# Kernel optimization log

Hardware: AMD Instinct MI355X
Metric: run time of the kernel (lower is better)

## Reference

```python
import jax, jax.numpy as jnp
import numpy as np

N = 100000   # nodes
E = 1600000  # edges (before self-loops)
G = 64       # graphs in batch
IN = 8
H = 4        # heads
EPS_BN = 1e-5

def setup_inputs() -> dict:
    key = jax.random.key(0)
    ks = jax.random.split(key, 30)
    def nrm(k, shape, s=0.1):
        return jax.random.normal(k, shape, dtype=jnp.float32) * s
    inp = {}
    inp['x'] = nrm(ks[0], (N, IN), 1.0)
    inp['edge_index'] = jax.random.randint(ks[1], (2, E), 0, N)
    inp['batch'] = jnp.sort(jax.random.randint(ks[2], (N,), 0, G))
    # GATConv 1: 8 -> 64, 4 heads (concat=False)
    inp['W1'] = nrm(ks[3], (IN, H * 64)); inp['aS1'] = nrm(ks[4], (H, 64)); inp['aD1'] = nrm(ks[5], (H, 64)); inp['b1'] = jnp.zeros((64,), jnp.float32)
    inp['g1'] = jnp.ones((64,), jnp.float32); inp['be1'] = jnp.zeros((64,), jnp.float32)
    # GATConv 2: 64 -> 64
    inp['W2'] = nrm(ks[6], (64, H * 64)); inp['aS2'] = nrm(ks[7], (H, 64)); inp['aD2'] = nrm(ks[8], (H, 64)); inp['b2'] = jnp.zeros((64,), jnp.float32)
    inp['g2'] = jnp.ones((64,), jnp.float32); inp['be2'] = jnp.zeros((64,), jnp.float32)
    # GATConv 3: 64 -> 32
    inp['W3'] = nrm(ks[9], (64, H * 32)); inp['aS3'] = nrm(ks[10], (H, 32)); inp['aD3'] = nrm(ks[11], (H, 32)); inp['b3'] = jnp.zeros((32,), jnp.float32)
    inp['g3'] = jnp.ones((32,), jnp.float32); inp['be3'] = jnp.zeros((32,), jnp.float32)
    # predictor MLP 32 -> 16 -> 1
    inp['Wp1'] = nrm(ks[12], (32, 16)); inp['bp1'] = jnp.zeros((16,), jnp.float32)
    inp['Wp2'] = nrm(ks[13], (16, 1)); inp['bp2'] = jnp.zeros((1,), jnp.float32)
    return inp

def gat_layer(x, src, dst, W, a_src, a_dst, bias, D):
    # x: [N, Fin]; src/dst: [E'] (self-loops included). PyG GATConv semantics.
    h = (x @ W).reshape(N, H, D)                       # [N,H,D]
    alpha_s = jnp.einsum('nhd,hd->nh', h, a_src)       # [N,H]
    alpha_d = jnp.einsum('nhd,hd->nh', h, a_dst)
    e = jax.nn.leaky_relu(alpha_s[src] + alpha_d[dst], 0.2)  # [E',H]
    # segment softmax over incoming edges of each target node
    m = jax.ops.segment_max(e, dst, num_segments=N)
    e = jnp.exp(e - m[dst])
    s = jax.ops.segment_sum(e, dst, num_segments=N)
    alpha = e / (s[dst] + 1e-16)                       # [E',H]
    out = jax.ops.segment_sum(h[src] * alpha[:, :, None], dst, num_segments=N)  # [N,H,D]
    return out.mean(axis=1) + bias                     # concat=False -> head mean

def batch_norm(x, gamma, beta):
    m = x.mean(0)
    v = x.var(0)
    return (x - m) * jax.lax.rsqrt(v + EPS_BN) * gamma + beta

def reference(x, edge_index, batch,
              W1, aS1, aD1, b1, g1, be1,
              W2, aS2, aD2, b2, g2, be2,
              W3, aS3, aD3, b3, g3, be3,
              Wp1, bp1, Wp2, bp2):
    loop = jnp.arange(N)
    src = jnp.concatenate([edge_index[0], loop])  # add self loops (PyG default)
    dst = jnp.concatenate([edge_index[1], loop])
    h = jax.nn.relu(gat_layer(x, src, dst, W1, aS1, aD1, b1, 64))
    h = batch_norm(h, g1, be1)
    h = jax.nn.relu(gat_layer(h, src, dst, W2, aS2, aD2, b2, 64))
    h = batch_norm(h, g2, be2)
    h = jax.nn.relu(gat_layer(h, src, dst, W3, aS3, aD3, b3, 32))
    h = batch_norm(h, g3, be3)
    # global mean pool over graphs
    cnt = jax.ops.segment_sum(jnp.ones((N,), h.dtype), batch, num_segments=G)
    pooled = jax.ops.segment_sum(h, batch, num_segments=G) / jnp.maximum(cnt, 1.0)[:, None]
    hid = jax.nn.relu(pooled @ Wp1 + bp1)
    return hid @ Wp2 + bp2  # [G,1]
```

## Files before the change

kernel.cpp:

```cpp
#include <hip/hip_runtime.h>
#include <hip/hip_fp16.h>

#define N_NODES 100000
#define N_EDGES 1600000
#define EP (N_EDGES + N_NODES)
#define NG 64
#define NH 4
#define POOL_NPB 256
#define BSHIFT 7
#define BNODES 128
#define NBUCK 782
#define BCAP 3072
#define BCHUNK 4096

static inline int cdiv(int a, int b) { return (a + b - 1) / b; }

typedef _Float16 half8 __attribute__((ext_vector_type(8)));
typedef float f32x4 __attribute__((ext_vector_type(4)));

__device__ __forceinline__ float lrelu(float x) { return x >= 0.f ? x : 0.2f * x; }

__global__ __launch_bounds__(256) void k_bucket(const int* __restrict__ ei,
                                                int* __restrict__ gCursor,
                                                unsigned int* __restrict__ pairs) {
  __shared__ int cnt[NBUCK];
  __shared__ int base[NBUCK];
  int tid = threadIdx.x;
  for (int b = tid; b < NBUCK; b += 256) cnt[b] = 0;
  __syncthreads();
  int e0 = blockIdx.x * BCHUNK;
  unsigned int stV[16];
  int stB[16];
#pragma unroll
  for (int i = 0; i < 16; i++) {
    int e = e0 + i * 256 + tid;
    stB[i] = -1;
    if (e < EP) {
      int d, s;
      if (e < N_EDGES) {
        d = __builtin_nontemporal_load(&ei[N_EDGES + e]);
        s = __builtin_nontemporal_load(&ei[e]);
      } else {
        d = s = e - N_EDGES;
      }
      int b = d >> BSHIFT;
      stV[i] = ((unsigned int)s << BSHIFT) | (unsigned int)(d & (BNODES - 1));
      stB[i] = b;
      atomicAdd(&cnt[b], 1);
    }
  }
  __syncthreads();
  for (int b = tid; b < NBUCK; b += 256) {
    base[b] = atomicAdd(&gCursor[b], cnt[b]);
    cnt[b] = 0;
  }
  __syncthreads();
#pragma unroll
  for (int i = 0; i < 16; i++) {
    if (stB[i] >= 0) {
      int r = atomicAdd(&cnt[stB[i]], 1);
      pairs[base[stB[i]] + r] = stV[i];
    }
  }
}

__global__ __launch_bounds__(1024) void k_bscan(const int* __restrict__ gCursor,
                                                int* __restrict__ bstart) {
  __shared__ int sh[1024];
  int t = threadIdx.x;
  int v = (t < NBUCK) ? (gCursor[t] - t * BCAP) : 0;
  sh[t] = v;
  __syncthreads();
  for (int off = 1; off < 1024; off <<= 1) {
    int add = (t >= off) ? sh[t - off] : 0;
    __syncthreads();
    sh[t] += add;
    __syncthreads();
  }
  if (t < NBUCK) {
    bstart[t] = sh[t] - v;
    if (t == NBUCK - 1) bstart[NBUCK] = sh[t];
  }
}

__global__ __launch_bounds__(256) void k_build(const unsigned int* __restrict__ pairs,
                                               const int* __restrict__ bstart,
                                               int* __restrict__ indptr, int* __restrict__ esrc) {
  __shared__ int cnt[BNODES];
  __shared__ int exc[BNODES];
  __shared__ int ptr[BNODES];
  __shared__ int eLds[BCAP];
  int b = blockIdx.x;
  int tid = threadIdx.x;
  int obase = bstart[b];
  int nE = bstart[b + 1] - obase;
  int pbase = b * BCAP;
  if (tid < BNODES) cnt[tid] = 0;
  __syncthreads();
  unsigned int stV[12];
#pragma unroll
  for (int i = 0; i < 12; i++) {
    int idx = i * 256 + tid;
    stV[i] = 0xFFFFFFFFu;
    if (idx < nE) {
      unsigned int v = pairs[pbase + idx];
      stV[i] = v;
      atomicAdd(&cnt[v & (BNODES - 1)], 1);
    }
  }
  __syncthreads();
  if (tid < BNODES) ptr[tid] = cnt[tid];
  __syncthreads();
  for (int off = 1; off < BNODES; off <<= 1) {
    int add = (tid < BNODES && tid >= off) ? ptr[tid - off] : 0;
    __syncthreads();
    if (tid < BNODES) ptr[tid] += add;
    __syncthreads();
  }
  if (tid < BNODES) {
    exc[tid] = ptr[tid] - cnt[tid];
    int n = (b << BSHIFT) + tid;
    if (n < N_NODES) indptr[n] = obase + exc[tid];
    cnt[tid] = 0;
  }
  if (b == NBUCK - 1 && tid == 0) indptr[N_NODES] = bstart[NBUCK];
  __syncthreads();
#pragma unroll
  for (int i = 0; i < 12; i++) {
    if (stV[i] != 0xFFFFFFFFu) {
      int ln = stV[i] & (BNODES - 1);
      int r = atomicAdd(&cnt[ln], 1);
      eLds[exc[ln] + r] = (int)(stV[i] >> BSHIFT);
    }
  }
  __syncthreads();
  for (int idx = tid; idx < nE; idx += 256) esrc[obase + idx] = eLds[idx];
}

template <int FIN, int D>
__device__ void wvec_impl(const float* __restrict__ W, const float* __restrict__ aS,
                          const float* __restrict__ aD, float* __restrict__ wS,
                          float* __restrict__ wD, int t) {
  if (t >= 4 * FIN) return;
  int h = t / FIN, k = t % FIN;
  float ss = 0.f, dd = 0.f;
  for (int d = 0; d < D; d++) {
    float w = W[k * (4 * D) + h * D + d];
    ss = fmaf(w, aS[h * D + d], ss);
    dd = fmaf(w, aD[h * D + d], dd);
  }
  wS[h * FIN + k] = ss;
  wD[h * FIN + k] = dd;
}

template <int D>
__device__ void wcvt_frag(const float* __restrict__ W, __half* __restrict__ wf, int frag, int l) {
  constexpr int NCT = D / 16;
  int kt = frag / NCT, ct = frag % NCT;
  half8 v;
#pragma unroll
  for (int j = 0; j < 8; j++) {
    int kk = kt * 32 + (l >> 4) * 8 + j;
    int k = kk >> 2, h = kk & 3;
    v[j] = (_Float16)W[k * (4 * D) + h * D + ct * 16 + (l & 15)];
  }
  *(half8*)(wf + (size_t)frag * 512 + l * 8) = v;
}

__global__ __launch_bounds__(256) void k_prep(const float* W1, const float* aS1, const float* aD1,
                                              const float* W2, const float* aS2, const float* aD2,
                                              const float* W3, const float* aS3, const float* aD3,
                                              float* wS1, float* wD1, float* wS2, float* wD2,
                                              float* wS3, float* wD3,
                                              __half* wf1, __half* wf2, __half* wf3,
                                              int* gCursor) {
  int b = blockIdx.x, t = threadIdx.x;
  int f = t >> 6, l = t & 63;
  if (b == 0) wvec_impl<8, 64>(W1, aS1, aD1, wS1, wD1, t);
  else if (b == 1) wvec_impl<64, 64>(W2, aS2, aD2, wS2, wD2, t);
  else if (b == 2) wvec_impl<64, 32>(W3, aS3, aD3, wS3, wD3, t);
  else if (b == 3) wcvt_frag<64>(W1, wf1, f, l);
  else if (b < 12) wcvt_frag<64>(W2, wf2, (b - 4) * 4 + f, l);
  else if (b < 16) wcvt_frag<32>(W3, wf3, (b - 12) * 4 + f, l);
  else {
    int idx = (b - 16) * 256 + t;
    if (idx < NBUCK) gCursor[idx] = idx * BCAP;
  }
}

__global__ void k_attdots1(const float* __restrict__ x, const float* __restrict__ wS,
                           const float* __restrict__ wD, float4* __restrict__ as4,
                           float4* __restrict__ ad4) {
  int n = blockIdx.x * blockDim.x + threadIdx.x;
  if (n >= N_NODES) return;
  float4 s = {0, 0, 0, 0}, d = {0, 0, 0, 0};
#pragma unroll
  for (int k = 0; k < 8; k++) {
    float xv = x[(size_t)n * 8 + k];
    s.x = fmaf(xv, wS[k], s.x);
    s.y = fmaf(xv, wS[8 + k], s.y);
    s.z = fmaf(xv, wS[16 + k], s.z);
    s.w = fmaf(xv, wS[24 + k], s.w);
    d.x = fmaf(xv, wD[k], d.x);
    d.y = fmaf(xv, wD[8 + k], d.y);
    d.z = fmaf(xv, wD[16 + k], d.z);
    d.w = fmaf(xv, wD[24 + k], d.w);
  }
  as4[n] = s;
  ad4[n] = d;
}

__global__ __launch_bounds__(256) void k_bnx(const float* __restrict__ tbuf,
                                             const float* __restrict__ scale,
                                             const float* __restrict__ shift,
                                             const float* __restrict__ wS,
                                             const float* __restrict__ wD,
                                             __half* __restrict__ xhat,
                                             float4* __restrict__ as4, float4* __restrict__ ad4) {
  int lane = threadIdx.x & 63;
  int n = blockIdx.x * 4 + (threadIdx.x >> 6);
  if (n >= N_NODES) return;
  float v = fmaf(tbuf[(size_t)n * 64 + lane], scale[lane], shift[lane]);
  xhat[(size_t)n * 64 + lane] = __float2half(v);
  float p0 = v * wS[lane], p1 = v * wS[64 + lane], p2 = v * wS[128 + lane], p3 = v * wS[192 + lane];
  float q0 = v * wD[lane], q1 = v * wD[64 + lane], q2 = v * wD[128 + lane], q3 = v * wD[192 + lane];
#pragma unroll
  for (int off = 32; off; off >>= 1) {
    p0 += __shfl_xor(p0, off); p1 += __shfl_xor(p1, off);
    p2 += __shfl_xor(p2, off); p3 += __shfl_xor(p3, off);
    q0 += __shfl_xor(q0, off); q1 += __shfl_xor(q1, off);
    q2 += __shfl_xor(q2, off); q3 += __shfl_xor(q3, off);
  }
  if (lane == 0) {
    as4[n] = make_float4(p0, p1, p2, p3);
    ad4[n] = make_float4(q0, q1, q2, q3);
  }
}

template <int DIN, typename TX, int GSH>
__global__ __launch_bounds__(256) void k_agg(const int* __restrict__ indptr,
                                             const int* __restrict__ esrc,
                                             const TX* __restrict__ xg,
                                             const float4* __restrict__ as4,
                                             const float4* __restrict__ ad4,
                                             __half* __restrict__ accO) {
  constexpr int GL = 1 << GSH;
  constexpr int NPW = 64 >> GSH;
  constexpr int DPL = DIN / GL;
  constexpr int SH = (sizeof(TX) == 2) ? 7 : 5;
  constexpr int WB = NPW * (GL + 1);
  __shared__ int sOff[4 * WB];
  __shared__ float4 sW[4 * WB];
  int tid = threadIdx.x;
  int lane = tid & 63;
  int wv = tid >> 6;
  int q = lane & (GL - 1);
  int g = lane >> GSH;
  int n = blockIdx.x * (4 * NPW) + wv * NPW + g;
  if (n >= N_NODES) return;
  int e0 = indptr[n], e1 = indptr[n + 1];
  float4 ad = ad4[n];
  int lbase = wv * WB + g * (GL + 1);
  const char* xb = (const char*)xg + q * DPL * (int)sizeof(TX);
  float s0 = 0.f, s1 = 0.f, s2 = 0.f, s3 = 0.f;
  float a[DPL][4];
#pragma unroll
  for (int d = 0; d < DPL; d++)
#pragma unroll
    for (int h = 0; h < 4; h++) a[d][h] = 0.f;

  for (int c = e0; c < e1; c += GL) {
    int nc = min(GL, e1 - c);
    float w0 = 0.f, w1 = 0.f, w2 = 0.f, w3 = 0.f;
    int sB = 0;
    if (q < nc) {
      int sidx = esrc[c + q];
      float4 av = as4[sidx];
      w0 = __expf(lrelu(av.x + ad.x));
      w1 = __expf(lrelu(av.y + ad.y));
      w2 = __expf(lrelu(av.z + ad.z));
      w3 = __expf(lrelu(av.w + ad.w));
      sB = sidx << SH;
    }
    s0 += w0; s1 += w1; s2 += w2; s3 += w3;
    sOff[lbase + q] = sB;
    sW[lbase + q] = make_float4(w0, w1, w2, w3);
    __builtin_amdgcn_wave_barrier();
    for (int i = 0; i < nc; ++i) {
      float4 w = sW[lbase + i];
      int ob = sOff[lbase + i];
      if constexpr (DPL == 4) {
        uint2 px = *(const uint2*)(xb + ob);
        float2 f01 = __half22float2(*(const __half2*)&px.x);
        float2 f23 = __half22float2(*(const __half2*)&px.y);
        a[0][0] = fmaf(w.x, f01.x, a[0][0]); a[0][1] = fmaf(w.y, f01.x, a[0][1]);
        a[0][2] = fmaf(w.z, f01.x, a[0][2]); a[0][3] = fmaf(w.w, f01.x, a[0][3]);
        a[1][0] = fmaf(w.x, f01.y, a[1][0]); a[1][1] = fmaf(w.y, f01.y, a[1][1]);
        a[1][2] = fmaf(w.z, f01.y, a[1][2]); a[1][3] = fmaf(w.w, f01.y, a[1][3]);
        a[2][0] = fmaf(w.x, f23.x, a[2][0]); a[2][1] = fmaf(w.y, f23.x, a[2][1]);
        a[2][2] = fmaf(w.z, f23.x, a[2][2]); a[2][3] = fmaf(w.w, f23.x, a[2][3]);
        a[3][0] = fmaf(w.x, f23.y, a[3][0]); a[3][1] = fmaf(w.y, f23.y, a[3][1]);
        a[3][2] = fmaf(w.z, f23.y, a[3][2]); a[3][3] = fmaf(w.w, f23.y, a[3][3]);
      } else {
        float xv = *(const float*)(xb + ob);
        a[0][0] = fmaf(w.x, xv, a[0][0]);
        a[0][1] = fmaf(w.y, xv, a[0][1]);
        a[0][2] = fmaf(w.z, xv, a[0][2]);
        a[0][3] = fmaf(w.w, xv, a[0][3]);
      }
    }
    __builtin_amdgcn_wave_barrier();
  }
#pragma unroll
  for (int off = 1; off < GL; off <<= 1) {
    s0 += __shfl_xor(s0, off);
    s1 += __shfl_xor(s1, off);
    s2 += __shfl_xor(s2, off);
    s3 += __shfl_xor(s3, off);
  }
  float r0 = 1.f / (s0 + 1e-16f), r1 = 1.f / (s1 + 1e-16f);
  float r2 = 1.f / (s2 + 1e-16f), r3 = 1.f / (s3 + 1e-16f);
  if constexpr (DPL == 4) {
    __half2 p[8];
#pragma unroll
    for (int d = 0; d < 4; d++) {
      p[2 * d] = __floats2half2_rn(a[d][0] * r0, a[d][1] * r1);
      p[2 * d + 1] = __floats2half2_rn(a[d][2] * r2, a[d][3] * r3);
    }
    uint4 lo = make_uint4(*(unsigned*)&p[0], *(unsigned*)&p[1], *(unsigned*)&p[2], *(unsigned*)&p[3]);
    uint4 hi = make_uint4(*(unsigned*)&p[4], *(unsigned*)&p[5], *(unsigned*)&p[6], *(unsigned*)&p[7]);
    *(uint4*)(accO + (size_t)n * 256 + q * 16) = lo;
    *(uint4*)(accO + (size_t)n * 256 + q * 16 + 8) = hi;
  } else {
    __half2 p01 = __floats2half2_rn(a[0][0] * r0, a[0][1] * r1);
    __half2 p23 = __floats2half2_rn(a[0][2] * r2, a[0][3] * r3);
    uint2 pk = make_uint2(*(unsigned*)&p01, *(unsigned*)&p23);
    *(uint2*)(accO + (size_t)n * 32 + q * 4) = pk;
  }
}

template <int DOUT, int NK>
__global__ __launch_bounds__(256) void k_post_mfma(const __half* __restrict__ accA,
                                                   const __half* __restrict__ wfrag,
                                                   const float* __restrict__ bias,
                                                   float* __restrict__ tbuf) {
  constexpr int NCT = DOUT / 16;
  constexpr int AS = NK * 32;
  int l = threadIdx.x & 63;
  int n0 = (blockIdx.x * 4 + (threadIdx.x >> 6)) * 16;
  int m = l & 15, kg = l >> 4;
  f32x4 c[NCT];
#pragma unroll
  for (int ct = 0; ct < NCT; ct++) c[ct] = (f32x4){0.f, 0.f, 0.f, 0.f};
#pragma unroll
  for (int kt = 0; kt < NK; kt++) {
    half8 a = *(const half8*)(accA + (size_t)(n0 + m) * AS + kt * 32 + kg * 8);
#pragma unroll
    for (int ct = 0; ct < NCT; ct++) {
      half8 b = *(const half8*)(wfrag + ((kt * NCT + ct) * 64 + l) * 8);
      c[ct] = __builtin_amdgcn_mfma_f32_16x16x32_f16(a, b, c[ct], 0, 0, 0);
    }
  }
#pragma unroll
  for (int ct = 0; ct < NCT; ct++) {
    float bv = bias[ct * 16 + m];
#pragma unroll
    for (int j = 0; j < 4; j++) {
      int n = n0 + kg * 4 + j;
      if (n < N_NODES) tbuf[(size_t)n * DOUT + ct * 16 + m] = fmaxf(fmaf(c[ct][j], 0.25f, bv), 0.f);
    }
  }
}

template <int C>
__global__ __launch_bounds__(256) void k_bnstat(const float* __restrict__ x, float* __restrict__ part) {
  const int RG = 256 / C;
  int col = threadIdx.x & (C - 1);
  int rg = threadIdx.x / C;
  int rows = (N_NODES + gridDim.x - 1) / gridDim.x;
  int r0 = blockIdx.x * rows;
  int r1 = min(N_NODES, r0 + rows);
  float s = 0.f, q = 0.f;
  for (int r = r0 + rg; r < r1; r += RG) {
    float v = x[(size_t)r * C + col];
    s += v;
    q = fmaf(v, v, q);
  }
  __shared__ float sh[512];
  sh[threadIdx.x] = s;
  sh[256 + threadIdx.x] = q;
  __syncthreads();
  for (int step = 128; step >= C; step >>= 1) {
    if (threadIdx.x < step) {
      sh[threadIdx.x] += sh[threadIdx.x + step];
      sh[256 + threadIdx.x] += sh[256 + threadIdx.x + step];
    }
    __syncthreads();
  }
  if (threadIdx.x < C) {
    part[blockIdx.x * 2 * C + threadIdx.x] = sh[threadIdx.x];
    part[blockIdx.x * 2 * C + C + threadIdx.x] = sh[256 + threadIdx.x];
  }
}

template <int C>
__global__ void k_bnfinal(const float* __restrict__ part, const float* __restrict__ g,
                          const float* __restrict__ be, float* __restrict__ scale,
                          float* __restrict__ shift) {
  int c = threadIdx.x;
  if (c >= C) return;
  float s = 0.f, q = 0.f;
  for (int b = 0; b < 256; b++) {
    s += part[b * 2 * C + c];
    q += part[b * 2 * C + C + c];
  }
  float mean = s / (float)N_NODES;
  float var = q / (float)N_NODES - mean * mean;
  float sc = g[c] * rsqrtf(var + 1e-5f);
  scale[c] = sc;
  shift[c] = be[c] - mean * sc;
}

__global__ __launch_bounds__(256) void k_pool(const float* __restrict__ f3,
                                              const int* __restrict__ batch,
                                              const float* __restrict__ scale,
                                              const float* __restrict__ shift,
                                              float* __restrict__ pool,
                                              float* __restrict__ cntg) {
  __shared__ float acc[NG][33];
  int t = threadIdx.x;
  for (int i = t; i < NG * 33; i += 256) ((float*)acc)[i] = 0.f;
  __syncthreads();
  int c = t & 31, rg = t >> 5;
  float sc = scale[c], sh = shift[c];
  int n0 = blockIdx.x * POOL_NPB;
  int n1 = min(N_NODES, n0 + POOL_NPB);
  float r = 0.f, rc = 0.f;
  int gcur = -1;
  for (int n = n0 + rg; n < n1; n += 8) {
    int g = batch[n];
    if (g != gcur) {
      if (gcur >= 0) {
        atomicAdd(&acc[gcur][c], r);
        if (c == 0) atomicAdd(&acc[gcur][32], rc);
      }
      gcur = g;
      r = 0.f;
      rc = 0.f;
    }
    r += fmaf(f3[(size_t)n * 32 + c], sc, sh);
    rc += 1.f;
  }
  if (gcur >= 0) {
    atomicAdd(&acc[gcur][c], r);
    if (c == 0) atomicAdd(&acc[gcur][32], rc);
  }
  __syncthreads();
  for (int i = t; i < NG * 32; i += 256) {
    int g = i >> 5, cc = i & 31;
    float v = acc[g][cc];
    if (v != 0.f) atomicAdd(&pool[i], v);
  }
  for (int g = t; g < NG; g += 256) {
    float v = acc[g][32];
    if (v != 0.f) atomicAdd(&cntg[g], v);
  }
}

__global__ void k_mlp(const float* __restrict__ pool, const float* __restrict__ cntg,
                      const float* __restrict__ Wp1, const float* __restrict__ bp1,
                      const float* __restrict__ Wp2, const float* __restrict__ bp2,
                      float* __restrict__ out) {
  int g = threadIdx.x;
  if (g >= NG) return;
  float inv = 1.f / fmaxf(cntg[g], 1.f);
  float p[32];
#pragma unroll
  for (int c = 0; c < 32; c++) p[c] = pool[g * 32 + c] * inv;
  float o = bp2[0];
  for (int j = 0; j < 16; j++) {
    float hsum = bp1[j];
#pragma unroll
    for (int c = 0; c < 32; c++) hsum = fmaf(p[c], Wp1[c * 16 + j], hsum);
    o = fmaf(fmaxf(hsum, 0.f), Wp2[j], o);
  }
  out[g] = o;
}

extern "C" void kernel_launch(void* const* d_in, const int* in_sizes, int n_in,
                              void* d_out, int out_size, void* d_ws, size_t ws_size,
                              hipStream_t stream) {
  const float* x = (const float*)d_in[0];
  const int* ei = (const int*)d_in[1];
  const int* batch = (const int*)d_in[2];
  const float* W1 = (const float*)d_in[3];
  const float* aS1 = (const float*)d_in[4];
  const float* aD1 = (const float*)d_in[5];
  const float* b1 = (const float*)d_in[6];
  const float* g1 = (const float*)d_in[7];
  const float* be1 = (const float*)d_in[8];
  const float* W2 = (const float*)d_in[9];
  const float* aS2 = (const float*)d_in[10];
  const float* aD2 = (const float*)d_in[11];
  const float* b2 = (const float*)d_in[12];
  const float* g2 = (const float*)d_in[13];
  const float* be2 = (const float*)d_in[14];
  const float* W3 = (const float*)d_in[15];
  const float* aS3 = (const float*)d_in[16];
  const float* aD3 = (const float*)d_in[17];
  const float* b3 = (const float*)d_in[18];
  const float* g3 = (const float*)d_in[19];
  const float* be3 = (const float*)d_in[20];
  const float* Wp1 = (const float*)d_in[21];
  const float* bp1 = (const float*)d_in[22];
  const float* Wp2 = (const float*)d_in[23];
  const float* bp2 = (const float*)d_in[24];
  float* out = (float*)d_out;

  size_t off = 0;
  auto alloc = [&](size_t bytes) -> void* {
    void* p = (char*)d_ws + off;
    off += (bytes + 255) & ~(size_t)255;
    return p;
  };
  float* pool = (float*)alloc((size_t)NG * 32 * 4);
  float* cntg = (float*)alloc((size_t)NG * 4);
  size_t zbytes = off;
  int* gCursor = (int*)alloc((size_t)NBUCK * 4);
  int* bstart = (int*)alloc((size_t)(NBUCK + 1) * 4);
  unsigned int* pairs = (unsigned int*)alloc((size_t)NBUCK * BCAP * 4);
  int* indptr = (int*)alloc((size_t)(N_NODES + 1) * 4);
  int* esrc = (int*)alloc((size_t)EP * 4);
  __half* xhat = (__half*)alloc((size_t)N_NODES * 64 * 2);
  __half* acc16 = (__half*)alloc((size_t)(N_NODES + 16) * 256 * 2);
  float* as_ = (float*)alloc((size_t)N_NODES * 16);
  float* ad_ = (float*)alloc((size_t)N_NODES * 16);
  float* tbuf = (float*)alloc((size_t)N_NODES * 64 * 4);
  float* part = (float*)alloc((size_t)256 * 128 * 4);
  float* scale = (float*)alloc(64 * 4);
  float* shift = (float*)alloc(64 * 4);
  float* wS1 = (float*)alloc(32 * 4);
  float* wD1 = (float*)alloc(32 * 4);
  float* wS2 = (float*)alloc(256 * 4);
  float* wD2 = (float*)alloc(256 * 4);
  float* wS3 = (float*)alloc(256 * 4);
  float* wD3 = (float*)alloc(256 * 4);
  __half* wf1 = (__half*)alloc((size_t)4 * 512 * 2);
  __half* wf2 = (__half*)alloc((size_t)32 * 512 * 2);
  __half* wf3 = (__half*)alloc((size_t)16 * 512 * 2);
  if (off > ws_size) return;

  hipMemsetAsync(pool, 0, zbytes, stream);

  k_prep<<<16 + cdiv(NBUCK, 256), 256, 0, stream>>>(W1, aS1, aD1, W2, aS2, aD2, W3, aS3, aD3,
                                                    wS1, wD1, wS2, wD2, wS3, wD3, wf1, wf2, wf3,
                                                    gCursor);
  k_bucket<<<cdiv(EP, BCHUNK), 256, 0, stream>>>(ei, gCursor, pairs);
  k_bscan<<<1, 1024, 0, stream>>>(gCursor, bstart);
  k_build<<<NBUCK, 256, 0, stream>>>(pairs, bstart, indptr, esrc);

  int npost = cdiv(N_NODES, 64);

  k_attdots1<<<cdiv(N_NODES, 256), 256, 0, stream>>>(x, wS1, wD1, (float4*)as_, (float4*)ad_);
  k_agg<8, float, 3><<<cdiv(N_NODES, 32), 256, 0, stream>>>(indptr, esrc, x, (const float4*)as_,
                                                            (const float4*)ad_, acc16);
  k_post_mfma<64, 1><<<npost, 256, 0, stream>>>(acc16, wf1, b1, tbuf);
  k_bnstat<64><<<256, 256, 0, stream>>>(tbuf, part);
  k_bnfinal<64><<<1, 64, 0, stream>>>(part, g1, be1, scale, shift);

  k_bnx<<<cdiv(N_NODES, 4), 256, 0, stream>>>(tbuf, scale, shift, wS2, wD2, xhat,
                                              (float4*)as_, (float4*)ad_);
  k_agg<64, __half, 4><<<cdiv(N_NODES, 16), 256, 0, stream>>>(indptr, esrc, xhat,
                                                              (const float4*)as_,
                                                              (const float4*)ad_, acc16);
  k_post_mfma<64, 8><<<npost, 256, 0, stream>>>(acc16, wf2, b2, tbuf);
  k_bnstat<64><<<256, 256, 0, stream>>>(tbuf, part);
  k_bnfinal<64><<<1, 64, 0, stream>>>(part, g2, be2, scale, shift);

  k_bnx<<<cdiv(N_NODES, 4), 256, 0, stream>>>(tbuf, scale, shift, wS3, wD3, xhat,
                                              (float4*)as_, (float4*)ad_);
  k_agg<64, __half, 4><<<cdiv(N_NODES, 16), 256, 0, stream>>>(indptr, esrc, xhat,
                                                              (const float4*)as_,
                                                              (const float4*)ad_, acc16);
  k_post_mfma<32, 8><<<npost, 256, 0, stream>>>(acc16, wf3, b3, tbuf);
  k_bnstat<32><<<256, 256, 0, stream>>>(tbuf, part);
  k_bnfinal<32><<<1, 32, 0, stream>>>(part, g3, be3, scale, shift);

  k_pool<<<cdiv(N_NODES, POOL_NPB), 256, 0, stream>>>(tbuf, batch, scale, shift, pool, cntg);
  k_mlp<<<1, 64, 0, stream>>>(pool, cntg, Wp1, bp1, Wp2, bp2, out);
}
```

Baseline: 454.6 us.

## Fuse layer 2/3 aggregation with MFMA projection through shared memory

Layers 2 and 3 now aggregate attention-weighted neighbour features into a 16-node tile in shared memory, then apply the MFMA weight projection, bias, head-mean and ReLU in the same kernel. This removes writing and re-reading the 256-wide fp16 aggregated buffer to global memory, along with two kernel launches. The cost is a block-wide barrier, so waves with low-degree nodes wait for the slowest node in the tile. Only 2 or 4 of the 4 waves do the MFMA step, and the extra shared memory may reduce occupancy.

```diff
diff --git a/kernel.cpp b/kernel.cpp
--- a/kernel.cpp
+++ b/kernel.cpp
@@ -237,38 +237,28 @@
   }
 }
 
-template <int DIN, typename TX, int GSH>
-__global__ __launch_bounds__(256) void k_agg(const int* __restrict__ indptr,
-                                             const int* __restrict__ esrc,
-                                             const TX* __restrict__ xg,
-                                             const float4* __restrict__ as4,
-                                             const float4* __restrict__ ad4,
-                                             __half* __restrict__ accO) {
-  constexpr int GL = 1 << GSH;
-  constexpr int NPW = 64 >> GSH;
-  constexpr int DPL = DIN / GL;
-  constexpr int SH = (sizeof(TX) == 2) ? 7 : 5;
-  constexpr int WB = NPW * (GL + 1);
+__global__ __launch_bounds__(256) void k_agg1(const int* __restrict__ indptr,
+                                              const int* __restrict__ esrc,
+                                              const float* __restrict__ xg,
+                                              const float4* __restrict__ as4,
+                                              const float4* __restrict__ ad4,
+                                              __half* __restrict__ accO) {
+  constexpr int GL = 8, NPW = 8, WB = NPW * (GL + 1);
   __shared__ int sOff[4 * WB];
   __shared__ float4 sW[4 * WB];
   int tid = threadIdx.x;
   int lane = tid & 63;
   int wv = tid >> 6;
   int q = lane & (GL - 1);
-  int g = lane >> GSH;
+  int g = lane >> 3;
   int n = blockIdx.x * (4 * NPW) + wv * NPW + g;
   if (n >= N_NODES) return;
   int e0 = indptr[n], e1 = indptr[n + 1];
   float4 ad = ad4[n];
   int lbase = wv * WB + g * (GL + 1);
-  const char* xb = (const char*)xg + q * DPL * (int)sizeof(TX);
+  const char* xb = (const char*)xg + q * 4;
   float s0 = 0.f, s1 = 0.f, s2 = 0.f, s3 = 0.f;
-  float a[DPL][4];
-#pragma unroll
-  for (int d = 0; d < DPL; d++)
-#pragma unroll
-    for (int h = 0; h < 4; h++) a[d][h] = 0.f;
-
+  float a0 = 0.f, a1 = 0.f, a2 = 0.f, a3 = 0.f;
   for (int c = e0; c < e1; c += GL) {
     int nc = min(GL, e1 - c);
     float w0 = 0.f, w1 = 0.f, w2 = 0.f, w3 = 0.f;
@@ -280,7 +270,7 @@
       w1 = __expf(lrelu(av.y + ad.y));
       w2 = __expf(lrelu(av.z + ad.z));
       w3 = __expf(lrelu(av.w + ad.w));
-      sB = sidx << SH;
+      sB = sidx << 5;
     }
     s0 += w0; s1 += w1; s2 += w2; s3 += w3;
     sOff[lbase + q] = sB;
@@ -289,25 +279,11 @@
     for (int i = 0; i < nc; ++i) {
       float4 w = sW[lbase + i];
       int ob = sOff[lbase + i];
-      if constexpr (DPL == 4) {
-        uint2 px = *(const uint2*)(xb + ob);
-        float2 f01 = __half22float2(*(const __half2*)&px.x);
-        float2 f23 = __half22float2(*(const __half2*)&px.y);
-        a[0][0] = fmaf(w.x, f01.x, a[0][0]); a[0][1] = fmaf(w.y, f01.x, a[0][1]);
-        a[0][2] = fmaf(w.z, f01.x, a[0][2]); a[0][3] = fmaf(w.w, f01.x, a[0][3]);
-        a[1][0] = fmaf(w.x, f01.y, a[1][0]); a[1][1] = fmaf(w.y, f01.y, a[1][1]);
-        a[1][2] = fmaf(w.z, f01.y, a[1][2]); a[1][3] = fmaf(w.w, f01.y, a[1][3]);
-        a[2][0] = fmaf(w.x, f23.x, a[2][0]); a[2][1] = fmaf(w.y, f23.x, a[2][1]);
-        a[2][2] = fmaf(w.z, f23.x, a[2][2]); a[2][3] = fmaf(w.w, f23.x, a[2][3]);
-        a[3][0] = fmaf(w.x, f23.y, a[3][0]); a[3][1] = fmaf(w.y, f23.y, a[3][1]);
-        a[3][2] = fmaf(w.z, f23.y, a[3][2]); a[3][3] = fmaf(w.w, f23.y, a[3][3]);
-      } else {
-        float xv = *(const float*)(xb + ob);
-        a[0][0] = fmaf(w.x, xv, a[0][0]);
-        a[0][1] = fmaf(w.y, xv, a[0][1]);
-        a[0][2] = fmaf(w.z, xv, a[0][2]);
-        a[0][3] = fmaf(w.w, xv, a[0][3]);
-      }
+      float xv = *(const float*)(xb + ob);
+      a0 = fmaf(w.x, xv, a0);
+      a1 = fmaf(w.y, xv, a1);
+      a2 = fmaf(w.z, xv, a2);
+      a3 = fmaf(w.w, xv, a3);
     }
     __builtin_amdgcn_wave_barrier();
   }
@@ -320,22 +296,114 @@
   }
   float r0 = 1.f / (s0 + 1e-16f), r1 = 1.f / (s1 + 1e-16f);
   float r2 = 1.f / (s2 + 1e-16f), r3 = 1.f / (s3 + 1e-16f);
-  if constexpr (DPL == 4) {
-    __half2 p[8];
-#pragma unroll
-    for (int d = 0; d < 4; d++) {
-      p[2 * d] = __floats2half2_rn(a[d][0] * r0, a[d][1] * r1);
-      p[2 * d + 1] = __floats2half2_rn(a[d][2] * r2, a[d][3] * r3);
-    }
-    uint4 lo = make_uint4(*(unsigned*)&p[0], *(unsigned*)&p[1], *(unsigned*)&p[2], *(unsigned*)&p[3]);
-    uint4 hi = make_uint4(*(unsigned*)&p[4], *(unsigned*)&p[5], *(unsigned*)&p[6], *(unsigned*)&p[7]);
-    *(uint4*)(accO + (size_t)n * 256 + q * 16) = lo;
-    *(uint4*)(accO + (size_t)n * 256 + q * 16 + 8) = hi;
-  } else {
-    __half2 p01 = __floats2half2_rn(a[0][0] * r0, a[0][1] * r1);
-    __half2 p23 = __floats2half2_rn(a[0][2] * r2, a[0][3] * r3);
-    uint2 pk = make_uint2(*(unsigned*)&p01, *(unsigned*)&p23);
-    *(uint2*)(accO + (size_t)n * 32 + q * 4) = pk;
+  __half2 p01 = __floats2half2_rn(a0 * r0, a1 * r1);
+  __half2 p23 = __floats2half2_rn(a2 * r2, a3 * r3);
+  uint2 pk = make_uint2(*(unsigned*)&p01, *(unsigned*)&p23);
+  *(uint2*)(accO + (size_t)n * 32 + q * 4) = pk;
+}
+
+template <int DOUT>
+__global__ __launch_bounds__(256) void k_aggp(const int* __restrict__ indptr,
+                                              const int* __restrict__ esrc,
+                                              const __half* __restrict__ xg,
+                                              const float4* __restrict__ as4,
+                                              const float4* __restrict__ ad4,
+                                              const __half* __restrict__ wfrag,
+                                              const float* __restrict__ bias,
+                                              float* __restrict__ tbuf) {
+  constexpr int NCT = DOUT / 16;
+  constexpr int GL = 16, NPW = 4, WB = NPW * (GL + 1);
+  __shared__ int sOff[4 * WB];
+  __shared__ float4 sW[4 * WB];
+  __shared__ __align__(16) __half aT[16 * 264];
+  int tid = threadIdx.x;
+  int lane = tid & 63;
+  int wv = tid >> 6;
+  int q = lane & 15;
+  int g = lane >> 4;
+  int row = wv * 4 + g;
+  int n = blockIdx.x * 16 + row;
+  int e0 = indptr[n], e1 = indptr[n + 1];
+  float4 ad = ad4[n];
+  int lbase = wv * WB + g * (GL + 1);
+  const char* xb = (const char*)xg + q * 8;
+  float s0 = 0.f, s1 = 0.f, s2 = 0.f, s3 = 0.f;
+  float a[4][4];
+#pragma unroll
+  for (int d = 0; d < 4; d++)
+#pragma unroll
+    for (int h = 0; h < 4; h++) a[d][h] = 0.f;
+
+  for (int c = e0; c < e1; c += GL) {
+    int nc = min(GL, e1 - c);
+    float w0 = 0.f, w1 = 0.f, w2 = 0.f, w3 = 0.f;
+    int sB = 0;
+    if (q < nc) {
+      int sidx = esrc[c + q];
+      float4 av = as4[sidx];
+      w0 = __expf(lrelu(av.x + ad.x));
+      w1 = __expf(lrelu(av.y + ad.y));
+      w2 = __expf(lrelu(av.z + ad.z));
+      w3 = __expf(lrelu(av.w + ad.w));
+      sB = sidx << 7;
+    }
+    s0 += w0; s1 += w1; s2 += w2; s3 += w3;
+    sOff[lbase + q] = sB;
+    sW[lbase + q] = make_float4(w0, w1, w2, w3);
+    __builtin_amdgcn_wave_barrier();
+    for (int i = 0; i < nc; ++i) {
+      float4 w = sW[lbase + i];
+      int ob = sOff[lbase + i];
+      uint2 px = *(const uint2*)(xb + ob);
+      float2 f01 = __half22float2(*(const __half2*)&px.x);
+      float2 f23 = __half22float2(*(const __half2*)&px.y);
+      a[0][0] = fmaf(w.x, f01.x, a[0][0]); a[0][1] = fmaf(w.y, f01.x, a[0][1]);
+      a[0][2] = fmaf(w.z, f01.x, a[0][2]); a[0][3] = fmaf(w.w, f01.x, a[0][3]);
+      a[1][0] = fmaf(w.x, f01.y, a[1][0]); a[1][1] = fmaf(w.y, f01.y, a[1][1]);
+      a[1][2] = fmaf(w.z, f01.y, a[1][2]); a[1][3] = fmaf(w.w, f01.y, a[1][3]);
+      a[2][0] = fmaf(w.x, f23.x, a[2][0]); a[2][1] = fmaf(w.y, f23.x, a[2][1]);
+      a[2][2] = fmaf(w.z, f23.x, a[2][2]); a[2][3] = fmaf(w.w, f23.x, a[2][3]);
+      a[3][0] = fmaf(w.x, f23.y, a[3][0]); a[3][1] = fmaf(w.y, f23.y, a[3][1]);
+      a[3][2] = fmaf(w.z, f23.y, a[3][2]); a[3][3] = fmaf(w.w, f23.y, a[3][3]);
+    }
+    __builtin_amdgcn_wave_barrier();
+  }
+#pragma unroll
+  for (int off = 1; off < GL; off <<= 1) {
+    s0 += __shfl_xor(s0, off);
+    s1 += __shfl_xor(s1, off);
+    s2 += __shfl_xor(s2, off);
+    s3 += __shfl_xor(s3, off);
+  }
+  float r0 = 1.f / (s0 + 1e-16f), r1 = 1.f / (s1 + 1e-16f);
+  float r2 = 1.f / (s2 + 1e-16f), r3 = 1.f / (s3 + 1e-16f);
+  __half2 p[8];
+#pragma unroll
+  for (int d = 0; d < 4; d++) {
+    p[2 * d] = __floats2half2_rn(a[d][0] * r0, a[d][1] * r1);
+    p[2 * d + 1] = __floats2half2_rn(a[d][2] * r2, a[d][3] * r3);
+  }
+  uint4 lo = make_uint4(*(unsigned*)&p[0], *(unsigned*)&p[1], *(unsigned*)&p[2], *(unsigned*)&p[3]);
+  uint4 hi = make_uint4(*(unsigned*)&p[4], *(unsigned*)&p[5], *(unsigned*)&p[6], *(unsigned*)&p[7]);
+  *(uint4*)&aT[row * 264 + q * 16] = lo;
+  *(uint4*)&aT[row * 264 + q * 16 + 8] = hi;
+  __syncthreads();
+  if (wv < NCT) {
+    int ct = wv;
+    int m = lane & 15, kg = lane >> 4;
+    f32x4 cacc = (f32x4){0.f, 0.f, 0.f, 0.f};
+#pragma unroll
+    for (int kt = 0; kt < 8; kt++) {
+      half8 av = *(const half8*)&aT[m * 264 + kt * 32 + kg * 8];
+      half8 bv = *(const half8*)(wfrag + ((kt * NCT + ct) * 64 + lane) * 8);
+      cacc = __builtin_amdgcn_mfma_f32_16x16x32_f16(av, bv, cacc, 0, 0, 0);
+    }
+    float bv = bias[ct * 16 + m];
+#pragma unroll
+    for (int j = 0; j < 4; j++) {
+      int nr = blockIdx.x * 16 + kg * 4 + j;
+      tbuf[(size_t)nr * DOUT + ct * 16 + m] = fmaxf(fmaf(cacc[j], 0.25f, bv), 0.f);
+    }
   }
 }
 
@@ -532,7 +600,7 @@
   int* indptr = (int*)alloc((size_t)(N_NODES + 1) * 4);
   int* esrc = (int*)alloc((size_t)EP * 4);
   __half* xhat = (__half*)alloc((size_t)N_NODES * 64 * 2);
-  __half* acc16 = (__half*)alloc((size_t)(N_NODES + 16) * 256 * 2);
+  __half* acc16 = (__half*)alloc((size_t)(N_NODES + 16) * 32 * 2);
   float* as_ = (float*)alloc((size_t)N_NODES * 16);
   float* ad_ = (float*)alloc((size_t)N_NODES * 16);
   float* tbuf = (float*)alloc((size_t)N_NODES * 64 * 4);
@@ -559,30 +627,24 @@
   k_bscan<<<1, 1024, 0, stream>>>(gCursor, bstart);
   k_build<<<NBUCK, 256, 0, stream>>>(pairs, bstart, indptr, esrc);
 
-  int npost = cdiv(N_NODES, 64);
-
   k_attdots1<<<cdiv(N_NODES, 256), 256, 0, stream>>>(x, wS1, wD1, (float4*)as_, (float4*)ad_);
-  k_agg<8, float, 3><<<cdiv(N_NODES, 32), 256, 0, stream>>>(indptr, esrc, x, (const float4*)as_,
-                                                            (const float4*)ad_, acc16);
-  k_post_mfma<64, 1><<<npost, 256, 0, stream>>>(acc16, wf1, b1, tbuf);
+  k_agg1<<<cdiv(N_NODES, 32), 256, 0, stream>>>(indptr, esrc, x, (const float4*)as_,
+                                                (const float4*)ad_, acc16);
+  k_post_mfma<64, 1><<<cdiv(N_NODES, 64), 256, 0, stream>>>(acc16, wf1, b1, tbuf);
   k_bnstat<64><<<256, 256, 0, stream>>>(tbuf, part);
   k_bnfinal<64><<<1, 64, 0, stream>>>(part, g1, be1, scale, shift);
 
   k_bnx<<<cdiv(N_NODES, 4), 256, 0, stream>>>(tbuf, scale, shift, wS2, wD2, xhat,
                                               (float4*)as_, (float4*)ad_);
-  k_agg<64, __half, 4><<<cdiv(N_NODES, 16), 256, 0, stream>>>(indptr, esrc, xhat,
-                                                              (const float4*)as_,
-                                                              (const float4*)ad_, acc16);
-  k_post_mfma<64, 8><<<npost, 256, 0, stream>>>(acc16, wf2, b2, tbuf);
+  k_aggp<64><<<N_NODES / 16, 256, 0, stream>>>(indptr, esrc, xhat, (const float4*)as_,
+                                               (const float4*)ad_, wf2, b2, tbuf);
   k_bnstat<64><<<256, 256, 0, stream>>>(tbuf, part);
   k_bnfinal<64><<<1, 64, 0, stream>>>(part, g2, be2, scale, shift);
 
   k_bnx<<<cdiv(N_NODES, 4), 256, 0, stream>>>(tbuf, scale, shift, wS3, wD3, xhat,
                                               (float4*)as_, (float4*)ad_);
-  k_agg<64, __half, 4><<<cdiv(N_NODES, 16), 256, 0, stream>>>(indptr, esrc, xhat,
-                                                              (const float4*)as_,
-                                                              (const float4*)ad_, acc16);
-  k_post_mfma<32, 8><<<npost, 256, 0, stream>>>(acc16, wf3, b3, tbuf);
+  k_aggp<32><<<N_NODES / 16, 256, 0, stream>>>(indptr, esrc, xhat, (const float4*)as_,
+                                               (const float4*)ad_, wf3, b3, tbuf);
   k_bnstat<32><<<256, 256, 0, stream>>>(tbuf, part);
   k_bnfinal<32><<<1, 32, 0, stream>>>(part, g3, be3, scale, shift);
 
```

New measurement: 427.6 us. 6.0% less time.
